# Optimization experiments

Measured on AMD Instinct MI355X. Metric: run time of the kernel, lower is better.

Reference implementation:

```python
import jax, jax.numpy as jnp
import numpy as np
import math

HIDDEN = 1024
HEADS = 16
HEAD_DIM = HIDDEN // HEADS
B, S = 2, 2048


def setup_inputs() -> dict:
    key = jax.random.key(0)
    ks = jax.random.split(key, 10)
    std = 1.0 / math.sqrt(HIDDEN)
    mk = lambda k: (jax.random.normal(k, (HIDDEN, HIDDEN), jnp.float32) * std)
    return {
        "hidden_states": jax.random.normal(ks[0], (B, S, HIDDEN), jnp.float32),
        "attention_mask": jnp.zeros((B, 1, 1, S), jnp.float32),
        "wq": mk(ks[1]), "bq": jnp.zeros((HIDDEN,), jnp.float32),
        "wk": mk(ks[2]), "bk": jnp.zeros((HIDDEN,), jnp.float32),
        "wv": mk(ks[3]), "bv": jnp.zeros((HIDDEN,), jnp.float32),
        "wo": mk(ks[4]), "bo": jnp.zeros((HIDDEN,), jnp.float32),
    }


def reference(hidden_states, attention_mask, wq, bq, wk, bk, wv, bv, wo, bo):
    b, s, _ = hidden_states.shape
    scale = math.sqrt(HEAD_DIM)
    # projections (torch Linear: x @ W.T + b); weights stored as [out, in]
    q = hidden_states @ wq.T + bq
    k = hidden_states @ wk.T + bk
    v = hidden_states @ wv.T + bv
    # [B, H, S, D]
    q = q.reshape(b, s, HEADS, HEAD_DIM).transpose(0, 2, 1, 3)
    k = k.reshape(b, s, HEADS, HEAD_DIM).transpose(0, 2, 1, 3)
    v = v.reshape(b, s, HEADS, HEAD_DIM).transpose(0, 2, 1, 3)
    scores = jnp.einsum("bhqd,bhkd->bhqk", q, k) / scale
    scores = scores + attention_mask  # broadcast [B,1,1,S]
    weights = jax.nn.softmax(scores, axis=-1)  # dropout = identity (eval)
    out = jnp.einsum("bhqk,bhkd->bhqd", weights, v)
    out = out.transpose(0, 2, 1, 3).reshape(b, s, HIDDEN)
    out = out @ wo.T + bo
    return out
```

## Files before the change

kernel.cpp:

```cpp
#include <hip/hip_runtime.h>
#include <hip/hip_bf16.h>

typedef __bf16 bf16_t;
typedef __bf16 bf16x8 __attribute__((ext_vector_type(8)));
typedef _Float16 f16x4 __attribute__((ext_vector_type(4)));
typedef _Float16 f16x8 __attribute__((ext_vector_type(8)));
typedef float f32x4 __attribute__((ext_vector_type(4)));

#define SEQ    2048
#define NH     16
#define HD     64
#define HIDDEN 1024
#define LOG2E  1.44269504f

#if __has_builtin(__builtin_amdgcn_exp2f)
#define EXP2F(x) __builtin_amdgcn_exp2f(x)
#else
#define EXP2F(x) exp2f(x)
#endif

__device__ __forceinline__ bf16_t to_bf16(float f) { return (bf16_t)f; }

__device__ __forceinline__ void async16(const void* g, void* l) {
    __builtin_amdgcn_global_load_lds((const __attribute__((address_space(1))) void*)g,
                                     (__attribute__((address_space(3))) void*)l, 16, 0, 0);
}

__global__ __launch_bounds__(256) void cvt_kernel(
    const float* __restrict__ s0, bf16_t* __restrict__ d0, int c0,
    const float* __restrict__ s1, bf16_t* __restrict__ d1, int c1,
    const float* __restrict__ s2, bf16_t* __restrict__ d2, int c2,
    const float* __restrict__ s3, bf16_t* __restrict__ d3, int c3,
    const float* __restrict__ s4, bf16_t* __restrict__ d4, int c4,
    const float* __restrict__ s5, float* __restrict__ d5)
{
    int blk = blockIdx.x;
    const float* s; bf16_t* d;
    if (blk < c0)              { s = s0; d = d0; }
    else if ((blk -= c0) < c1) { s = s1; d = d1; }
    else if ((blk -= c1) < c2) { s = s2; d = d2; }
    else if ((blk -= c2) < c3) { s = s3; d = d3; }
    else if ((blk -= c3) < c4) { s = s4; d = d4; }
    else {
        blk -= c4;
        const size_t base = (size_t)blk * 2048 + threadIdx.x * 8;
        float4 a = *(const float4*)&s5[base];
        float4 b = *(const float4*)&s5[base + 4];
        a.x *= LOG2E; a.y *= LOG2E; a.z *= LOG2E; a.w *= LOG2E;
        b.x *= LOG2E; b.y *= LOG2E; b.z *= LOG2E; b.w *= LOG2E;
        *(float4*)&d5[base] = a;
        *(float4*)&d5[base + 4] = b;
        return;
    }
    const size_t base = (size_t)blk * 2048 + threadIdx.x * 8;
    const float4 a = *(const float4*)&s[base];
    const float4 b = *(const float4*)&s[base + 4];
    bf16x8 o;
    o[0] = (bf16_t)a.x; o[1] = (bf16_t)a.y; o[2] = (bf16_t)a.z; o[3] = (bf16_t)a.w;
    o[4] = (bf16_t)b.x; o[5] = (bf16_t)b.y; o[6] = (bf16_t)b.z; o[7] = (bf16_t)b.w;
    *(bf16x8*)&d[base] = o;
}

__global__ __launch_bounds__(256, 3) void qkv_kernel(
    const bf16_t* __restrict__ X,
    const bf16_t* __restrict__ wq, const bf16_t* __restrict__ wk, const bf16_t* __restrict__ wv,
    const float* __restrict__ bq, const float* __restrict__ bk, const float* __restrict__ bv,
    bf16_t* __restrict__ qws, bf16_t* __restrict__ kws, _Float16* __restrict__ vws)
{
    __shared__ __align__(16) bf16_t Sh[16384];
    const int z = blockIdx.z;
    const bf16_t* Wsel = (z == 0) ? wq : (z == 1) ? wk : wv;
    const float*  bsel = (z == 0) ? bq : (z == 1) ? bk : bv;
    const int m0 = blockIdx.y * 128, n0 = blockIdx.x * 128;

    const int t = threadIdx.x, lane = t & 63, w = t >> 6;
    const int w0 = w & 1, w1 = w >> 1, l15 = lane & 15, q4 = lane >> 4;

    f32x4 acc[4][4];
#pragma unroll
    for (int i = 0; i < 4; i++)
#pragma unroll
        for (int j = 0; j < 4; j++) acc[i][j] = f32x4{0.f, 0.f, 0.f, 0.f};

    auto stage = [&](int kt, int buf) {
#pragma unroll
        for (int j = 0; j < 2; j++) {
            const int s = j * 256 + t;
            const int row = s >> 2, c = (s & 3) ^ (row & 3);
            const int lb = buf * 8192 + (j * 256 + w * 64) * 8;
            async16(&X[(size_t)(m0 + row) * HIDDEN + kt + c * 8], &Sh[lb]);
            async16(&Wsel[(size_t)(n0 + row) * HIDDEN + kt + c * 8], &Sh[lb + 4096]);
        }
    };
    stage(0, 0);

    for (int it = 0; it < 32; it++) {
        const int cur = it & 1;
        __syncthreads();
        if (it < 31) stage((it + 1) * 32, cur ^ 1);
        const bf16_t* As = &Sh[cur * 8192];
        const bf16_t* Bs = &Sh[cur * 8192 + 4096];
        bf16x8 af[4];
#pragma unroll
        for (int ti = 0; ti < 4; ti++) {
            const int ra = w0 * 64 + ti * 16 + l15;
            af[ti] = *(const bf16x8*)&As[ra * 32 + (q4 ^ (ra & 3)) * 8];
        }
#pragma unroll
        for (int tj = 0; tj < 4; tj++) {
            const int rb = w1 * 64 + tj * 16 + l15;
            const bf16x8 bfr = *(const bf16x8*)&Bs[rb * 32 + (q4 ^ (rb & 3)) * 8];
#pragma unroll
            for (int ti = 0; ti < 4; ti++)
                acc[ti][tj] = __builtin_amdgcn_mfma_f32_16x16x32_bf16(af[ti], bfr, acc[ti][tj], 0, 0, 0);
        }
    }
    __syncthreads();

    if (z < 2) {
#pragma unroll
        for (int tj = 0; tj < 4; tj++) {
            const int n = w1 * 64 + tj * 16 + l15;
            const float bb = bsel[n0 + n];
            const int ch = (n >> 3), sub = n & 7;
#pragma unroll
            for (int ti = 0; ti < 4; ti++)
#pragma unroll
                for (int r = 0; r < 4; r++) {
                    const int m = w0 * 64 + ti * 16 + q4 * 4 + r;
                    Sh[m * 128 + ((ch ^ (m & 15)) << 3) + sub] = to_bf16(acc[ti][tj][r] + bb);
                }
        }
        __syncthreads();
        bf16_t* dst = (z == 0) ? qws : kws;
#pragma unroll
        for (int i = 0; i < 8; i++) {
            const int g = i * 256 + t;
            const int row = g >> 4, c = g & 15;
            const bf16x8 vv = *(const bf16x8*)&Sh[row * 128 + ((c ^ (row & 15)) << 3)];
            *(bf16x8*)&dst[(size_t)(m0 + row) * HIDDEN + n0 + c * 8] = vv;
        }
    } else {
        _Float16* Vt = (_Float16*)Sh;
#pragma unroll
        for (int tj = 0; tj < 4; tj++) {
            const int n = w1 * 64 + tj * 16 + l15;
            const float bb = bsel[n0 + n];
#pragma unroll
            for (int ti = 0; ti < 4; ti++) {
                const int mb = w0 * 64 + ti * 16 + q4 * 4;
                f16x4 v;
#pragma unroll
                for (int r = 0; r < 4; r++) v[r] = (_Float16)(acc[ti][tj][r] + bb);
                *(f16x4*)&Vt[n * 128 + (((mb >> 3) ^ (n & 15)) << 3) + (mb & 7)] = v;
            }
        }
        __syncthreads();
        const int b = m0 >> 11, sbase = m0 & (SEQ - 1);
#pragma unroll
        for (int i = 0; i < 8; i++) {
            const int g = i * 256 + t;
            const int row = g >> 4, c = g & 15;
            const int sA = (c >> 2) * 32 + (c & 3) * 4;
            const int sB = sA + 16;
            const f16x4 va = *(const f16x4*)&Vt[row * 128 + (((sA >> 3) ^ (row & 15)) << 3) + (sA & 7)];
            const f16x4 vb = *(const f16x4*)&Vt[row * 128 + (((sB >> 3) ^ (row & 15)) << 3) + (sB & 7)];
            f16x8 vv;
            vv[0] = va[0]; vv[1] = va[1]; vv[2] = va[2]; vv[3] = va[3];
            vv[4] = vb[0]; vv[5] = vb[1]; vv[6] = vb[2]; vv[7] = vb[3];
            const int d = (n0 + row) & 63, hh = (n0 + row) >> 6;
            *(f16x8*)&vws[(((size_t)b * NH + hh) * HD + d) * SEQ + sbase + c * 8] = vv;
        }
    }
}

__global__ __launch_bounds__(256, 4) void attn_kernel(
    const bf16_t* __restrict__ Qw, const bf16_t* __restrict__ Kw,
    const _Float16* __restrict__ Vtw, const float* __restrict__ Msc,
    bf16_t* __restrict__ Ow)
{
    __shared__ __align__(16) bf16_t Tiles[2][2][64 * 64];

    const int t = threadIdx.x, lane = t & 63, w = t >> 6;
    const int l15 = lane & 15, q4 = lane >> 4;
    const int lid = blockIdx.x;
    const int c8 = lid & 7, jx = lid >> 3;
    const int bh = c8 * 4 + (jx >> 5);
    const int q0 = (jx & 31) * 64;
    const int b = bh >> 4, h = bh & 15;

    const bf16_t* Qh = Qw + (size_t)b * SEQ * HIDDEN + h * HD;
    const bf16_t* Kh = Kw + (size_t)b * SEQ * HIDDEN + h * HD;
    const _Float16* Vh = Vtw + (size_t)bh * HD * SEQ;
    const float* Mrow = Msc + (size_t)b * SEQ;

    const int qrow = q0 + w * 16 + l15;
    bf16x8 qf[2];
#pragma unroll
    for (int ks = 0; ks < 2; ks++)
        qf[ks] = *(const bf16x8*)&Qh[(size_t)qrow * HIDDEN + ks * 32 + q4 * 8];

    f32x4 oacc[4];
#pragma unroll
    for (int nb = 0; nb < 4; nb++) oacc[nb] = f32x4{0.f, 0.f, 0.f, 0.f};
    f32x4 osum = f32x4{0.f, 0.f, 0.f, 0.f};

    f16x8 vone;
#pragma unroll
    for (int i = 0; i < 8; i++) vone[i] = (_Float16)1.0f;

    int koff[8];
#pragma unroll
    for (int cb = 0; cb < 4; cb++)
#pragma unroll
        for (int ks = 0; ks < 2; ks++) {
            const int rk = cb * 16 + l15;
            koff[cb * 2 + ks] = rk * 64 + (((ks * 4 + q4) ^ (rk & 7)) << 3);
        }
    int voff[8];
#pragma unroll
    for (int t2 = 0; t2 < 2; t2++)
#pragma unroll
        for (int nb = 0; nb < 4; nb++) {
            const int rv = nb * 16 + l15;
            voff[t2 * 4 + nb] = rv * 64 + (((t2 * 4 + q4) ^ (rv & 7)) << 3);
        }

    const int rs0 = t >> 3, cs0 = (t & 7) ^ (rs0 & 7);
    const int rs1 = 32 + rs0, cs1 = (t & 7) ^ (rs1 & 7);
    const bf16_t*   Kp0 = Kh + (size_t)rs0 * HIDDEN + cs0 * 8;
    const bf16_t*   Kp1 = Kh + (size_t)rs1 * HIDDEN + cs1 * 8;
    const _Float16* Vp0 = Vh + (size_t)rs0 * SEQ + cs0 * 8;
    const _Float16* Vp1 = Vh + (size_t)rs1 * SEQ + cs1 * 8;
    const int db0 = (0 * 256 + w * 64) * 8, db1 = (1 * 256 + w * 64) * 8;

    auto stageKV = [&](int it, int buf) {
        const int kt = it * 64;
        bf16_t*   Kd = &Tiles[buf][0][0];
        _Float16* Vd = (_Float16*)&Tiles[buf][1][0];
        async16(Kp0 + (size_t)kt * HIDDEN, &Kd[db0]);
        async16(Vp0 + kt,                  &Vd[db0]);
        async16(Kp1 + (size_t)kt * HIDDEN, &Kd[db1]);
        async16(Vp1 + kt,                  &Vd[db1]);
    };

    auto iterBody = [&](int it, int buf) {
        __syncthreads();
        if (it < 31) stageKV(it + 1, buf ^ 1);

        const bf16_t*   Ksh = &Tiles[buf][0][0];
        const _Float16* Vsh = (const _Float16*)&Tiles[buf][1][0];

        float4 mv4[4];
#pragma unroll
        for (int cb = 0; cb < 4; cb++) mv4[cb] = *(const float4*)&Mrow[it * 64 + cb * 16 + q4 * 4];

        f32x4 sa[4];
#pragma unroll
        for (int cb = 0; cb < 4; cb++) sa[cb] = f32x4{0.f, 0.f, 0.f, 0.f};
        __builtin_amdgcn_s_setprio(1);
#pragma unroll
        for (int cb = 0; cb < 4; cb++)
#pragma unroll
            for (int ks = 0; ks < 2; ks++) {
                const bf16x8 kf = *(const bf16x8*)&Ksh[koff[cb * 2 + ks]];
                sa[cb] = __builtin_amdgcn_mfma_f32_16x16x32_bf16(kf, qf[ks], sa[cb], 0, 0, 0);
            }
        __builtin_amdgcn_s_setprio(0);

        f16x8 pa[2];
#pragma unroll
        for (int cb = 0; cb < 4; cb++) {
            const float4 mv = mv4[cb];
            const float mk[4] = {mv.x, mv.y, mv.z, mv.w};
#pragma unroll
            for (int r = 0; r < 4; r++) {
                const float p = EXP2F(fmaf(sa[cb][r], 0.125f * LOG2E, mk[r]));
                pa[cb >> 1][(cb & 1) * 4 + r] = (_Float16)p;
            }
        }

        __builtin_amdgcn_s_setprio(1);
#pragma unroll
        for (int t2 = 0; t2 < 2; t2++) {
#pragma unroll
            for (int nb = 0; nb < 4; nb++) {
                const f16x8 vf = *(const f16x8*)&Vsh[voff[t2 * 4 + nb]];
                oacc[nb] = __builtin_amdgcn_mfma_f32_16x16x32_f16(pa[t2], vf, oacc[nb], 0, 0, 0);
            }
            osum = __builtin_amdgcn_mfma_f32_16x16x32_f16(pa[t2], vone, osum, 0, 0, 0);
        }
        __builtin_amdgcn_s_setprio(0);
    };

    stageKV(0, 0);
#pragma unroll 1
    for (int it2 = 0; it2 < 16; it2++) {
        iterBody(it2 * 2, 0);
        iterBody(it2 * 2 + 1, 1);
    }

    float inv[4];
#pragma unroll
    for (int r = 0; r < 4; r++) inv[r] = 1.f / osum[r];
#pragma unroll
    for (int r = 0; r < 4; r++) {
        const int srow = q0 + w * 16 + q4 * 4 + r;
#pragma unroll
        for (int nb = 0; nb < 4; nb++)
            Ow[((size_t)b * SEQ + srow) * HIDDEN + h * HD + nb * 16 + l15] =
                to_bf16(oacc[nb][r] * inv[r]);
    }
}

__global__ __launch_bounds__(256, 2) void oproj_kernel(
    const bf16_t* __restrict__ A, const bf16_t* __restrict__ Wo,
    const float* __restrict__ bo, float* __restrict__ Out)
{
    __shared__ __align__(16) bf16_t Sh[12288];
    const int m0 = blockIdx.y * 64, n0 = blockIdx.x * 128;
    const int t = threadIdx.x, lane = t & 63, w = t >> 6;
    const int l15 = lane & 15, q4 = lane >> 4;

    f32x4 acc[4][2];
#pragma unroll
    for (int i = 0; i < 4; i++)
#pragma unroll
        for (int j = 0; j < 2; j++) acc[i][j] = f32x4{0.f, 0.f, 0.f, 0.f};

    auto stage = [&](int kt, int buf) {
        {
            const int row = t >> 2, c = (t & 3) ^ (row & 3);
            async16(&A[(size_t)(m0 + row) * HIDDEN + kt + c * 8], &Sh[buf * 6144 + w * 64 * 8]);
        }
#pragma unroll
        for (int j = 0; j < 2; j++) {
            const int s = j * 256 + t;
            const int row = s >> 2, c = (s & 3) ^ (row & 3);
            async16(&Wo[(size_t)(n0 + row) * HIDDEN + kt + c * 8],
                    &Sh[buf * 6144 + 2048 + (j * 256 + w * 64) * 8]);
        }
    };
    stage(0, 0);

    for (int it = 0; it < 32; it++) {
        const int cur = it & 1;
        __syncthreads();
        if (it < 31) stage((it + 1) * 32, cur ^ 1);
        const bf16_t* As = &Sh[cur * 6144];
        const bf16_t* Bs = &Sh[cur * 6144 + 2048];
        bf16x8 af[4];
#pragma unroll
        for (int ti = 0; ti < 4; ti++) {
            const int ra = ti * 16 + l15;
            af[ti] = *(const bf16x8*)&As[ra * 32 + (q4 ^ (ra & 3)) * 8];
        }
#pragma unroll
        for (int tj = 0; tj < 2; tj++) {
            const int rb = w * 32 + tj * 16 + l15;
            const bf16x8 bfr = *(const bf16x8*)&Bs[rb * 32 + (q4 ^ (rb & 3)) * 8];
#pragma unroll
            for (int ti = 0; ti < 4; ti++)
                acc[ti][tj] = __builtin_amdgcn_mfma_f32_16x16x32_bf16(bfr, af[ti], acc[ti][tj], 0, 0, 0);
        }
    }

#pragma unroll
    for (int tj = 0; tj < 2; tj++) {
        const int nb4 = n0 + w * 32 + tj * 16 + q4 * 4;
        const float4 bb = *(const float4*)&bo[nb4];
#pragma unroll
        for (int ti = 0; ti < 4; ti++) {
            const int m = m0 + ti * 16 + l15;
            float4 ov;
            ov.x = acc[ti][tj][0] + bb.x;
            ov.y = acc[ti][tj][1] + bb.y;
            ov.z = acc[ti][tj][2] + bb.z;
            ov.w = acc[ti][tj][3] + bb.w;
            *(float4*)&Out[(size_t)m * HIDDEN + nb4] = ov;
        }
    }
}

extern "C" void kernel_launch(void* const* d_in, const int* in_sizes, int n_in,
                              void* d_out, int out_size, void* d_ws, size_t ws_size,
                              hipStream_t stream) {
    const float* X   = (const float*)d_in[0];
    const float* msk = (const float*)d_in[1];
    const float* wq  = (const float*)d_in[2];
    const float* bq  = (const float*)d_in[3];
    const float* wk  = (const float*)d_in[4];
    const float* bk  = (const float*)d_in[5];
    const float* wv  = (const float*)d_in[6];
    const float* bv  = (const float*)d_in[7];
    const float* wo  = (const float*)d_in[8];
    const float* bo  = (const float*)d_in[9];
    float* out = (float*)d_out;

    const size_t NELT = (size_t)2 * SEQ * HIDDEN;
    const size_t WELT = (size_t)HIDDEN * HIDDEN;
    bf16_t*    xbf = (bf16_t*)d_ws;
    bf16_t*    qws = xbf + NELT;
    bf16_t*    kws = qws + NELT;
    _Float16*  vws = (_Float16*)(kws + NELT);
    bf16_t*    aws = xbf;
    bf16_t*    wqb = (bf16_t*)d_out;
    bf16_t*    wkb = wqb + WELT;
    bf16_t*    wvb = wkb + WELT;
    bf16_t*    wob = wvb + WELT;
    float*     mws = (float*)(wob + WELT);

    cvt_kernel<<<dim3(2048 + 4 * 512 + 2), dim3(256), 0, stream>>>(
        X, xbf, 2048, wq, wqb, 512, wk, wkb, 512, wv, wvb, 512, wo, wob, 512,
        msk, mws);
    qkv_kernel<<<dim3(8, 32, 3), dim3(256), 0, stream>>>(
        xbf, wqb, wkb, wvb, bq, bk, bv, qws, kws, vws);
    attn_kernel<<<dim3(1024), dim3(256), 0, stream>>>(qws, kws, vws, mws, aws);
    oproj_kernel<<<dim3(8, 64), dim3(256), 0, stream>>>(aws, wob, bo, out);
}
```

Before: 190.7 us.

## Split attention keys across wave pairs with 32-row query tiles and LDS reduction

Each wave now handles 32 query rows and half of every 64-key tile, instead of 16 query rows over the full tile. Each K fragment read from LDS feeds two MFMAs and each V fragment feeds two, which halves the per-wave LDS reads per MFMA. The two key-half partial accumulators and row sums are combined through LDS at the end. This adds a final reduction step and two extra barriers, and raises accumulator register pressure, which could hurt occupancy.

Measured after the change: 195.5 us. 2.5% more time.

```diff
diff --git a/kernel.cpp b/kernel.cpp
--- a/kernel.cpp
+++ b/kernel.cpp
@@ -12,6 +12,7 @@
 #define HD     64
 #define HIDDEN 1024
 #define LOG2E  1.44269504f
+#define CSTR   41
 
 #if __has_builtin(__builtin_amdgcn_exp2f)
 #define EXP2F(x) __builtin_amdgcn_exp2f(x)
@@ -183,6 +184,7 @@
 
     const int t = threadIdx.x, lane = t & 63, w = t >> 6;
     const int l15 = lane & 15, q4 = lane >> 4;
+    const int wq = w & 1, kp = w >> 1;
     const int lid = blockIdx.x;
     const int c8 = lid & 7, jx = lid >> 3;
     const int bh = c8 * 4 + (jx >> 5);
@@ -194,37 +196,40 @@
     const _Float16* Vh = Vtw + (size_t)bh * HD * SEQ;
     const float* Mrow = Msc + (size_t)b * SEQ;
 
-    const int qrow = q0 + w * 16 + l15;
-    bf16x8 qf[2];
-#pragma unroll
-    for (int ks = 0; ks < 2; ks++)
-        qf[ks] = *(const bf16x8*)&Qh[(size_t)qrow * HIDDEN + ks * 32 + q4 * 8];
-
-    f32x4 oacc[4];
-#pragma unroll
-    for (int nb = 0; nb < 4; nb++) oacc[nb] = f32x4{0.f, 0.f, 0.f, 0.f};
-    f32x4 osum = f32x4{0.f, 0.f, 0.f, 0.f};
+    bf16x8 qf[2][2];
+#pragma unroll
+    for (int qb = 0; qb < 2; qb++)
+#pragma unroll
+        for (int ks = 0; ks < 2; ks++)
+            qf[qb][ks] = *(const bf16x8*)&Qh[(size_t)(q0 + wq * 32 + qb * 16 + l15) * HIDDEN + ks * 32 + q4 * 8];
+
+    f32x4 oacc[2][4];
+#pragma unroll
+    for (int qb = 0; qb < 2; qb++)
+#pragma unroll
+        for (int db = 0; db < 4; db++) oacc[qb][db] = f32x4{0.f, 0.f, 0.f, 0.f};
+    f32x4 osum[2];
+    osum[0] = f32x4{0.f, 0.f, 0.f, 0.f};
+    osum[1] = f32x4{0.f, 0.f, 0.f, 0.f};
 
     f16x8 vone;
 #pragma unroll
     for (int i = 0; i < 8; i++) vone[i] = (_Float16)1.0f;
 
-    int koff[8];
-#pragma unroll
-    for (int cb = 0; cb < 4; cb++)
+    int koff[4];
+#pragma unroll
+    for (int cb = 0; cb < 2; cb++)
 #pragma unroll
         for (int ks = 0; ks < 2; ks++) {
-            const int rk = cb * 16 + l15;
+            const int rk = kp * 32 + cb * 16 + l15;
             koff[cb * 2 + ks] = rk * 64 + (((ks * 4 + q4) ^ (rk & 7)) << 3);
         }
-    int voff[8];
-#pragma unroll
-    for (int t2 = 0; t2 < 2; t2++)
-#pragma unroll
-        for (int nb = 0; nb < 4; nb++) {
-            const int rv = nb * 16 + l15;
-            voff[t2 * 4 + nb] = rv * 64 + (((t2 * 4 + q4) ^ (rv & 7)) << 3);
-        }
+    int voff[4];
+#pragma unroll
+    for (int db = 0; db < 4; db++) {
+        const int rv = db * 16 + l15;
+        voff[db] = rv * 64 + (((kp * 4 + q4) ^ (rv & 7)) << 3);
+    }
 
     const int rs0 = t >> 3, cs0 = (t & 7) ^ (rs0 & 7);
     const int rs1 = 32 + rs0, cs1 = (t & 7) ^ (rs1 & 7);
@@ -251,45 +256,50 @@
         const bf16_t*   Ksh = &Tiles[buf][0][0];
         const _Float16* Vsh = (const _Float16*)&Tiles[buf][1][0];
 
-        float4 mv4[4];
-#pragma unroll
-        for (int cb = 0; cb < 4; cb++) mv4[cb] = *(const float4*)&Mrow[it * 64 + cb * 16 + q4 * 4];
-
-        f32x4 sa[4];
-#pragma unroll
-        for (int cb = 0; cb < 4; cb++) sa[cb] = f32x4{0.f, 0.f, 0.f, 0.f};
+        float4 mv4[2];
+#pragma unroll
+        for (int cb = 0; cb < 2; cb++)
+            mv4[cb] = *(const float4*)&Mrow[it * 64 + kp * 32 + cb * 16 + q4 * 4];
+
+        f32x4 sa[2][2];
+#pragma unroll
+        for (int qb = 0; qb < 2; qb++)
+#pragma unroll
+            for (int cb = 0; cb < 2; cb++) sa[qb][cb] = f32x4{0.f, 0.f, 0.f, 0.f};
         __builtin_amdgcn_s_setprio(1);
 #pragma unroll
-        for (int cb = 0; cb < 4; cb++)
+        for (int cb = 0; cb < 2; cb++)
 #pragma unroll
             for (int ks = 0; ks < 2; ks++) {
                 const bf16x8 kf = *(const bf16x8*)&Ksh[koff[cb * 2 + ks]];
-                sa[cb] = __builtin_amdgcn_mfma_f32_16x16x32_bf16(kf, qf[ks], sa[cb], 0, 0, 0);
+                sa[0][cb] = __builtin_amdgcn_mfma_f32_16x16x32_bf16(kf, qf[0][ks], sa[0][cb], 0, 0, 0);
+                sa[1][cb] = __builtin_amdgcn_mfma_f32_16x16x32_bf16(kf, qf[1][ks], sa[1][cb], 0, 0, 0);
             }
         __builtin_amdgcn_s_setprio(0);
 
         f16x8 pa[2];
 #pragma unroll
-        for (int cb = 0; cb < 4; cb++) {
+        for (int cb = 0; cb < 2; cb++) {
             const float4 mv = mv4[cb];
             const float mk[4] = {mv.x, mv.y, mv.z, mv.w};
 #pragma unroll
-            for (int r = 0; r < 4; r++) {
-                const float p = EXP2F(fmaf(sa[cb][r], 0.125f * LOG2E, mk[r]));
-                pa[cb >> 1][(cb & 1) * 4 + r] = (_Float16)p;
-            }
+            for (int qb = 0; qb < 2; qb++)
+#pragma unroll
+                for (int r = 0; r < 4; r++) {
+                    const float p = EXP2F(fmaf(sa[qb][cb][r], 0.125f * LOG2E, mk[r]));
+                    pa[qb][cb * 4 + r] = (_Float16)p;
+                }
         }
 
         __builtin_amdgcn_s_setprio(1);
 #pragma unroll
-        for (int t2 = 0; t2 < 2; t2++) {
-#pragma unroll
-            for (int nb = 0; nb < 4; nb++) {
-                const f16x8 vf = *(const f16x8*)&Vsh[voff[t2 * 4 + nb]];
-                oacc[nb] = __builtin_amdgcn_mfma_f32_16x16x32_f16(pa[t2], vf, oacc[nb], 0, 0, 0);
-            }
-            osum = __builtin_amdgcn_mfma_f32_16x16x32_f16(pa[t2], vone, osum, 0, 0, 0);
-        }
+        for (int db = 0; db < 4; db++) {
+            const f16x8 vf = *(const f16x8*)&Vsh[voff[db]];
+            oacc[0][db] = __builtin_amdgcn_mfma_f32_16x16x32_f16(pa[0], vf, oacc[0][db], 0, 0, 0);
+            oacc[1][db] = __builtin_amdgcn_mfma_f32_16x16x32_f16(pa[1], vf, oacc[1][db], 0, 0, 0);
+        }
+        osum[0] = __builtin_amdgcn_mfma_f32_16x16x32_f16(pa[0], vone, osum[0], 0, 0, 0);
+        osum[1] = __builtin_amdgcn_mfma_f32_16x16x32_f16(pa[1], vone, osum[1], 0, 0, 0);
         __builtin_amdgcn_s_setprio(0);
     };
 
@@ -299,17 +309,42 @@
         iterBody(it2 * 2, 0);
         iterBody(it2 * 2 + 1, 1);
     }
-
-    float inv[4];
-#pragma unroll
-    for (int r = 0; r < 4; r++) inv[r] = 1.f / osum[r];
-#pragma unroll
-    for (int r = 0; r < 4; r++) {
-        const int srow = q0 + w * 16 + q4 * 4 + r;
-#pragma unroll
-        for (int nb = 0; nb < 4; nb++)
-            Ow[((size_t)b * SEQ + srow) * HIDDEN + h * HD + nb * 16 + l15] =
-                to_bf16(oacc[nb][r] * inv[r]);
+    __syncthreads();
+
+    float* Cb = (float*)&Tiles[0][0][0];
+    const int crow = (wq * 64 + lane) * CSTR;
+    if (kp == 1) {
+#pragma unroll
+        for (int qb = 0; qb < 2; qb++) {
+#pragma unroll
+            for (int db = 0; db < 4; db++)
+                *(f32x4*)&Cb[crow + (qb * 4 + db) * 4] = oacc[qb][db];
+            *(f32x4*)&Cb[crow + 32 + qb * 4] = osum[qb];
+        }
+    }
+    __syncthreads();
+    if (kp == 0) {
+#pragma unroll
+        for (int qb = 0; qb < 2; qb++) {
+#pragma unroll
+            for (int db = 0; db < 4; db++)
+                oacc[qb][db] += *(const f32x4*)&Cb[crow + (qb * 4 + db) * 4];
+            osum[qb] += *(const f32x4*)&Cb[crow + 32 + qb * 4];
+        }
+#pragma unroll
+        for (int qb = 0; qb < 2; qb++) {
+            float inv[4];
+#pragma unroll
+            for (int r = 0; r < 4; r++) inv[r] = 1.f / osum[qb][r];
+#pragma unroll
+            for (int r = 0; r < 4; r++) {
+                const int srow = q0 + wq * 32 + qb * 16 + q4 * 4 + r;
+#pragma unroll
+                for (int db = 0; db < 4; db++)
+                    Ow[((size_t)b * SEQ + srow) * HIDDEN + h * HD + db * 16 + l15] =
+                        to_bf16(oacc[qb][db][r] * inv[r]);
+            }
+        }
     }
 }
 
```
